# Kernel tuning notes

Measured on AMD Instinct MI355X. Metric: run time of the kernel, lower is better.

Reference implementation:

```python
import jax, jax.numpy as jnp
import numpy as np

B, S, D = 2, 2048, 2048
H = 16
HD = D // H  # 128


def setup_inputs() -> dict:
    key = jax.random.key(0)
    ks = jax.random.split(key, 9)
    s = 1.0 / np.sqrt(D)
    return {
        "hidden_states": jax.random.normal(ks[0], (B, S, D), dtype=jnp.float32),
        "Wq": jax.random.normal(ks[1], (D, D), dtype=jnp.float32) * s,
        "bq": jnp.zeros((D,), dtype=jnp.float32),
        "Wk": jax.random.normal(ks[2], (D, D), dtype=jnp.float32) * s,
        "bk": jnp.zeros((D,), dtype=jnp.float32),
        "Wv": jax.random.normal(ks[3], (D, D), dtype=jnp.float32) * s,
        "bv": jnp.zeros((D,), dtype=jnp.float32),
        "Wo": jax.random.normal(ks[4], (D, D), dtype=jnp.float32) * s,
        "bo": jnp.zeros((D,), dtype=jnp.float32),
    }


def reference(hidden_states, Wq, bq, Wk, bk, Wv, bv, Wo, bo):
    x = hidden_states
    # linear projections (torch Linear: x @ W.T + b)
    q = x @ Wq.T + bq
    k = x @ Wk.T + bk
    v = x @ Wv.T + bv
    # [B, S, H, HD] -> [B, H, S, HD]
    q = q.reshape(B, S, H, HD).transpose(0, 2, 1, 3)
    k = k.reshape(B, S, H, HD).transpose(0, 2, 1, 3)
    v = v.reshape(B, S, H, HD).transpose(0, 2, 1, 3)
    q = q / jnp.sqrt(jnp.float32(HD))
    # scores [B, H, S, S]
    scores = jnp.einsum("bhqd,bhkd->bhqk", q, k)
    causal = jnp.triu(jnp.full((S, S), -jnp.inf, dtype=scores.dtype), k=1)
    scores = scores + causal
    attn = jax.nn.softmax(scores, axis=-1)
    out = jnp.einsum("bhqk,bhkd->bhqd", attn, v)
    out = out.transpose(0, 2, 1, 3).reshape(B, S, D)
    return out @ Wo.T + bo
```

## Files before the change

kernel.cpp:

```cpp
#include <hip/hip_runtime.h>
#include <stdint.h>

#define S_LEN 2048
#define DMODEL 2048
#define NHEAD 16
#define HDIM 128

typedef __attribute__((ext_vector_type(8))) short short8;
typedef __attribute__((ext_vector_type(4))) float floatx4;

__device__ __forceinline__ unsigned short f2b(float f) {
  union { float f; unsigned u; } v; v.f = f;
  unsigned r = v.u + 0x7FFFu + ((v.u >> 16) & 1u);
  return (unsigned short)(r >> 16);
}

__device__ __forceinline__ void load_lds16(const unsigned short* g, unsigned short* l) {
  __builtin_amdgcn_global_load_lds((const __attribute__((address_space(1))) void*)g,
                                   (__attribute__((address_space(3))) void*)l, 16, 0, 0);
}

__global__ __launch_bounds__(256) void cvt_all(const float* __restrict__ x,
                                               const float* __restrict__ Wq, const float* __restrict__ Wk,
                                               const float* __restrict__ Wv, const float* __restrict__ Wo,
                                               unsigned short* __restrict__ xb,
                                               unsigned short* __restrict__ Wqb, unsigned short* __restrict__ Wkb,
                                               unsigned short* __restrict__ Wvb, unsigned short* __restrict__ Wob) {
  const size_t idx = (size_t)blockIdx.x * 256 + threadIdx.x;
  const int y = blockIdx.y;
  const float4* s; ushort4* d;
  if (y == 0)      { s = (const float4*)x;               d = (ushort4*)xb; }
  else if (y == 1) { s = (const float4*)x + (1u << 20);  d = (ushort4*)xb + (1u << 20); }
  else if (y == 2) { s = (const float4*)Wq;              d = (ushort4*)Wqb; }
  else if (y == 3) { s = (const float4*)Wk;              d = (ushort4*)Wkb; }
  else if (y == 4) { s = (const float4*)Wv;              d = (ushort4*)Wvb; }
  else             { s = (const float4*)Wo;              d = (ushort4*)Wob; }
  float4 f = s[idx];
  ushort4 o;
  o.x = f2b(f.x); o.y = f2b(f.y); o.z = f2b(f.z); o.w = f2b(f.w);
  d[idx] = o;
}

template <int MODE>
__global__ __launch_bounds__(256)
void gemm_bt(const unsigned short* __restrict__ A, const unsigned short* __restrict__ Bw,
             const float* __restrict__ bias, void* __restrict__ Cout,
             int M, int N, int K, float scale) {
  __shared__ unsigned short As[128 * 64];
  __shared__ unsigned short Bs[128 * 64];
  const int t = threadIdx.x;
  const int lane = t & 63, wave = t >> 6;
  const int quad = lane >> 4, lc = lane & 15;
  const int wm = wave >> 1, wn = wave & 1;
  const int m0 = blockIdx.y * 128, n0 = blockIdx.x * 128;

  const int srow = lane >> 3;
  const int skoff = ((lane & 7) ^ srow) * 8;
  const unsigned short* Ag[4];
  const unsigned short* Bg[4];
  unsigned short* Al[4];
  unsigned short* Bl[4];
#pragma unroll
  for (int i = 0; i < 4; i++) {
    int c = wave * 4 + i;
    Ag[i] = A + (size_t)(m0 + c * 8 + srow) * K + skoff;
    Bg[i] = Bw + (size_t)(n0 + c * 8 + srow) * K + skoff;
    Al[i] = &As[c * 512 + lane * 8];
    Bl[i] = &Bs[c * 512 + lane * 8];
  }

  int koff[2];
#pragma unroll
  for (int ks = 0; ks < 2; ks++) koff[ks] = ((ks * 4 + quad) ^ (lc & 7)) * 8;

  floatx4 acc[4][4] = {};

  for (int kt = 0; kt < K; kt += 64) {
    if (kt) __syncthreads();
#pragma unroll
    for (int i = 0; i < 4; i++) {
      load_lds16(Ag[i] + kt, Al[i]);
      load_lds16(Bg[i] + kt, Bl[i]);
    }
    __syncthreads();
#pragma unroll
    for (int ks = 0; ks < 2; ks++) {
      short8 av[4], bv[4];
#pragma unroll
      for (int mt = 0; mt < 4; mt++)
        av[mt] = *(const short8*)&As[(wm * 64 + mt * 16 + lc) * 64 + koff[ks]];
#pragma unroll
      for (int nt = 0; nt < 4; nt++)
        bv[nt] = *(const short8*)&Bs[(wn * 64 + nt * 16 + lc) * 64 + koff[ks]];
#pragma unroll
      for (int mt = 0; mt < 4; mt++)
#pragma unroll
        for (int nt = 0; nt < 4; nt++)
          acc[mt][nt] = __builtin_amdgcn_mfma_f32_16x16x32_bf16(av[mt], bv[nt], acc[mt][nt], 0, 0, 0);
    }
  }

#pragma unroll
  for (int nt = 0; nt < 4; nt++) {
    const int col = n0 + wn * 64 + nt * 16 + lc;
    const float bcol = bias[col];
#pragma unroll
    for (int mt = 0; mt < 4; mt++) {
      const int row0 = m0 + wm * 64 + mt * 16 + quad * 4;
      if (MODE == 1) {
        ushort4 o;
        o.x = f2b((acc[mt][nt][0] + bcol) * scale);
        o.y = f2b((acc[mt][nt][1] + bcol) * scale);
        o.z = f2b((acc[mt][nt][2] + bcol) * scale);
        o.w = f2b((acc[mt][nt][3] + bcol) * scale);
        int b = row0 >> 11;
        int s = row0 & (S_LEN - 1);
        *(ushort4*)&((unsigned short*)Cout)[((size_t)(b * DMODEL + col)) * S_LEN + s] = o;
      } else {
#pragma unroll
        for (int r = 0; r < 4; r++) {
          float v = (acc[mt][nt][r] + bcol) * scale;
          if (MODE == 2)
            ((float*)Cout)[(size_t)(row0 + r) * N + col] = v;
          else
            ((unsigned short*)Cout)[(size_t)(row0 + r) * N + col] = f2b(v);
        }
      }
    }
  }
}

__global__ __launch_bounds__(256, 2)
void attn_fwd(const unsigned short* __restrict__ Qg, const unsigned short* __restrict__ Kg,
              const unsigned short* __restrict__ Vtg, unsigned short* __restrict__ Og) {
  __shared__ unsigned short Ks[64 * 128];
  __shared__ unsigned short Vs[128 * 64];
  __shared__ unsigned short Ps[128 * 64];

  const int t = threadIdx.x;
  const int lane = t & 63, w = t >> 6;
  const int quad = lane >> 4, lc = lane & 15;
  const int y = blockIdx.y;
  const int tile = (y < 16) ? (int)blockIdx.x : 15 - (int)blockIdx.x;
  const int b = y >> 4, h = y & 15;
  const size_t qkbase = (size_t)b * S_LEN * DMODEL + h * HDIM;
  const size_t vtbase = ((size_t)(b * DMODEL + h * HDIM)) * S_LEN;
  const int q0 = tile * 128;
  const int wrow = q0 + w * 32;

  short8 aq[2][4];
#pragma unroll
  for (int pm = 0; pm < 2; pm++)
#pragma unroll
    for (int ks = 0; ks < 4; ks++)
      aq[pm][ks] = *(const short8*)&Qg[qkbase + (size_t)(wrow + pm * 16 + lc) * DMODEL + ks * 32 + quad * 8];

  const unsigned short* kga[4];
  const unsigned short* vga[4];
  unsigned short* klds[4];
  unsigned short* vlds[4];
#pragma unroll
  for (int i = 0; i < 4; i++) {
    int c = w * 4 + i;
    int krow = 4 * c + (lane >> 4);
    int kch = (lane & 15) ^ (krow & 15);
    kga[i] = Kg + qkbase + (size_t)krow * DMODEL + kch * 8;
    klds[i] = &Ks[c * 512 + lane * 8];
    int vrow = 8 * c + (lane >> 3);
    int vch = (lane & 7) ^ (vrow & 7);
    vga[i] = Vtg + vtbase + (size_t)vrow * S_LEN + vch * 8;
    vlds[i] = &Vs[c * 512 + lane * 8];
  }

  floatx4 oacc[2][8] = {};
  float m_run[2][4], l_run[2][4];
#pragma unroll
  for (int pm = 0; pm < 2; pm++)
#pragma unroll
    for (int r = 0; r < 4; r++) { m_run[pm][r] = -1e30f; l_run[pm][r] = 0.f; }

  const int kiters = 2 * tile + 2;
  for (int kb = 0; kb < kiters; kb++) {
    const int k0 = kb * 64;
    if (kb) __syncthreads();
#pragma unroll
    for (int i = 0; i < 4; i++) {
      load_lds16(kga[i] + (size_t)k0 * DMODEL, klds[i]);
      load_lds16(vga[i] + k0, vlds[i]);
    }
    __syncthreads();

    if (k0 <= wrow + 31) {
      floatx4 sacc[2][4] = {};
#pragma unroll
      for (int ks = 0; ks < 4; ks++) {
        short8 bk[4];
#pragma unroll
        for (int nt = 0; nt < 4; nt++) {
          int n = nt * 16 + lc;
          bk[nt] = *(const short8*)&Ks[n * 128 + (((ks * 4 + quad) ^ (n & 15)) * 8)];
        }
#pragma unroll
        for (int pm = 0; pm < 2; pm++)
#pragma unroll
          for (int nt = 0; nt < 4; nt++)
            sacc[pm][nt] = __builtin_amdgcn_mfma_f32_16x16x32_bf16(aq[pm][ks], bk[nt], sacc[pm][nt], 0, 0, 0);
      }

      float mx[2][4];
#pragma unroll
      for (int pm = 0; pm < 2; pm++)
#pragma unroll
        for (int r = 0; r < 4; r++) mx[pm][r] = -1e30f;
      if (k0 + 63 > wrow) {
#pragma unroll
        for (int pm = 0; pm < 2; pm++)
#pragma unroll
          for (int nt = 0; nt < 4; nt++) {
            int col = k0 + nt * 16 + lc;
#pragma unroll
            for (int r = 0; r < 4; r++) {
              if (col > wrow + pm * 16 + quad * 4 + r) sacc[pm][nt][r] = -1e30f;
              mx[pm][r] = fmaxf(mx[pm][r], sacc[pm][nt][r]);
            }
          }
      } else {
#pragma unroll
        for (int pm = 0; pm < 2; pm++)
#pragma unroll
          for (int nt = 0; nt < 4; nt++)
#pragma unroll
            for (int r = 0; r < 4; r++) mx[pm][r] = fmaxf(mx[pm][r], sacc[pm][nt][r]);
      }
#pragma unroll
      for (int off = 1; off < 16; off <<= 1)
#pragma unroll
        for (int pm = 0; pm < 2; pm++)
#pragma unroll
          for (int r = 0; r < 4; r++) mx[pm][r] = fmaxf(mx[pm][r], __shfl_xor(mx[pm][r], off));

      float alpha[2][4];
#pragma unroll
      for (int pm = 0; pm < 2; pm++)
#pragma unroll
        for (int r = 0; r < 4; r++) {
          float mnew = fmaxf(m_run[pm][r], mx[pm][r]);
          alpha[pm][r] = __expf(m_run[pm][r] - mnew);
          m_run[pm][r] = mnew;
          l_run[pm][r] *= alpha[pm][r];
        }
#pragma unroll
      for (int pm = 0; pm < 2; pm++)
#pragma unroll
        for (int nt = 0; nt < 4; nt++) {
          int chs = ((nt * 2 + (lc >> 3)) * 8) + (lc & 7);
#pragma unroll
          for (int r = 0; r < 4; r++) {
            float p = __expf(sacc[pm][nt][r] - m_run[pm][r]);
            l_run[pm][r] += p;
            int row = w * 32 + pm * 16 + quad * 4 + r;
            int sw = (((nt * 2 + (lc >> 3)) ^ (row & 7)) * 8) + (lc & 7);
            Ps[row * 64 + sw] = f2b(p);
          }
          (void)chs;
        }

#pragma unroll
      for (int pm = 0; pm < 2; pm++)
#pragma unroll
        for (int nt8 = 0; nt8 < 8; nt8++)
#pragma unroll
          for (int r = 0; r < 4; r++) oacc[pm][nt8][r] *= alpha[pm][r];

#pragma unroll
      for (int ks = 0; ks < 2; ks++) {
        short8 ap[2];
#pragma unroll
        for (int pm = 0; pm < 2; pm++) {
          int m = w * 32 + pm * 16 + lc;
          ap[pm] = *(const short8*)&Ps[m * 64 + (((ks * 4 + quad) ^ (m & 7)) * 8)];
        }
#pragma unroll
        for (int nt8 = 0; nt8 < 8; nt8++) {
          int n = nt8 * 16 + lc;
          short8 bv = *(const short8*)&Vs[n * 64 + (((ks * 4 + quad) ^ (n & 7)) * 8)];
#pragma unroll
          for (int pm = 0; pm < 2; pm++)
            oacc[pm][nt8] = __builtin_amdgcn_mfma_f32_16x16x32_bf16(ap[pm], bv, oacc[pm][nt8], 0, 0, 0);
        }
      }
    }
  }

#pragma unroll
  for (int off = 1; off < 16; off <<= 1)
#pragma unroll
    for (int pm = 0; pm < 2; pm++)
#pragma unroll
      for (int r = 0; r < 4; r++) l_run[pm][r] += __shfl_xor(l_run[pm][r], off);
#pragma unroll
  for (int pm = 0; pm < 2; pm++)
#pragma unroll
    for (int r = 0; r < 4; r++) {
      float inv = 1.f / l_run[pm][r];
      size_t obase = ((size_t)(b * S_LEN + wrow + pm * 16 + quad * 4 + r)) * DMODEL + h * HDIM;
#pragma unroll
      for (int nt8 = 0; nt8 < 8; nt8++)
        Og[obase + nt8 * 16 + lc] = f2b(oacc[pm][nt8][r] * inv);
    }
}

extern "C" void kernel_launch(void* const* d_in, const int* in_sizes, int n_in,
                              void* d_out, int out_size, void* d_ws, size_t ws_size,
                              hipStream_t stream) {
  const float* x  = (const float*)d_in[0];
  const float* Wq = (const float*)d_in[1];
  const float* bq = (const float*)d_in[2];
  const float* Wk = (const float*)d_in[3];
  const float* bk = (const float*)d_in[4];
  const float* Wv = (const float*)d_in[5];
  const float* bv = (const float*)d_in[6];
  const float* Wo = (const float*)d_in[7];
  const float* bo = (const float*)d_in[8];

  const int M = 2 * S_LEN;
  const int N = DMODEL, K = DMODEL;

  char* w = (char*)d_ws;
  unsigned short* xb  = (unsigned short*)(w);
  unsigned short* Wqb = (unsigned short*)(w + (size_t)16 * (1 << 20));
  unsigned short* Wkb = (unsigned short*)(w + (size_t)24 * (1 << 20));
  unsigned short* Wvb = (unsigned short*)(w + (size_t)32 * (1 << 20));
  unsigned short* Wob = (unsigned short*)(w + (size_t)40 * (1 << 20));
  unsigned short* Qb  = (unsigned short*)(w + (size_t)48 * (1 << 20));
  unsigned short* Kb  = (unsigned short*)(w + (size_t)64 * (1 << 20));
  unsigned short* Vtb = (unsigned short*)(w + (size_t)80 * (1 << 20));
  unsigned short* Ob  = (unsigned short*)(w + (size_t)96 * (1 << 20));

  cvt_all<<<dim3(4096, 6), 256, 0, stream>>>(x, Wq, Wk, Wv, Wo, xb, Wqb, Wkb, Wvb, Wob);

  dim3 gg(N / 128, M / 128);
  const float qscale = 0.08838834764831843f;
  gemm_bt<0><<<gg, 256, 0, stream>>>(xb, Wqb, bq, Qb, M, N, K, qscale);
  gemm_bt<0><<<gg, 256, 0, stream>>>(xb, Wkb, bk, Kb, M, N, K, 1.f);
  gemm_bt<1><<<gg, 256, 0, stream>>>(xb, Wvb, bv, Vtb, M, N, K, 1.f);

  attn_fwd<<<dim3(16, 32), 256, 0, stream>>>(Qb, Kb, Vtb, Ob);

  gemm_bt<2><<<gg, 256, 0, stream>>>(Ob, Wob, bo, d_out, M, N, K, 1.f);
}
```

Before: 411.3 us.

## Double-buffer K tiles and overlap V load with QK^T in attention

The attention kernel now double-buffers the K tile in shared memory and prefetches the next K block while computing QK^T on the current one. The V tile load is issued at the start of each iteration and waited on with a partial vmcnt wait plus a barrier just before the PV product. Softmax switches to exp2, with log2(e) folded into the Q projection scale. This aims to hide global-to-LDS load latency behind the MFMA work and to cut exp cost, at the price of more LDS use, which may reduce occupancy, and of a hand-written waitcnt whose count has to be right.

```diff
diff --git a/kernel.cpp b/kernel.cpp
--- a/kernel.cpp
+++ b/kernel.cpp
@@ -133,7 +133,7 @@
 __global__ __launch_bounds__(256, 2)
 void attn_fwd(const unsigned short* __restrict__ Qg, const unsigned short* __restrict__ Kg,
               const unsigned short* __restrict__ Vtg, unsigned short* __restrict__ Og) {
-  __shared__ unsigned short Ks[64 * 128];
+  __shared__ unsigned short Ks[2][64 * 128];
   __shared__ unsigned short Vs[128 * 64];
   __shared__ unsigned short Ps[128 * 64];
 
@@ -157,19 +157,16 @@
 
   const unsigned short* kga[4];
   const unsigned short* vga[4];
-  unsigned short* klds[4];
-  unsigned short* vlds[4];
+  int kloff[4], vloff[4];
 #pragma unroll
   for (int i = 0; i < 4; i++) {
     int c = w * 4 + i;
     int krow = 4 * c + (lane >> 4);
-    int kch = (lane & 15) ^ (krow & 15);
-    kga[i] = Kg + qkbase + (size_t)krow * DMODEL + kch * 8;
-    klds[i] = &Ks[c * 512 + lane * 8];
+    kga[i] = Kg + qkbase + (size_t)krow * DMODEL + ((lane & 15) ^ (krow & 15)) * 8;
+    kloff[i] = c * 512 + lane * 8;
     int vrow = 8 * c + (lane >> 3);
-    int vch = (lane & 7) ^ (vrow & 7);
-    vga[i] = Vtg + vtbase + (size_t)vrow * S_LEN + vch * 8;
-    vlds[i] = &Vs[c * 512 + lane * 8];
+    vga[i] = Vtg + vtbase + (size_t)vrow * S_LEN + ((lane & 7) ^ (vrow & 7)) * 8;
+    vloff[i] = c * 512 + lane * 8;
   }
 
   floatx4 oacc[2][8] = {};
@@ -180,25 +177,38 @@
     for (int r = 0; r < 4; r++) { m_run[pm][r] = -1e30f; l_run[pm][r] = 0.f; }
 
   const int kiters = 2 * tile + 2;
+
+#pragma unroll
+  for (int i = 0; i < 4; i++) load_lds16(kga[i], &Ks[0][kloff[i]]);
+
   for (int kb = 0; kb < kiters; kb++) {
     const int k0 = kb * 64;
-    if (kb) __syncthreads();
-#pragma unroll
-    for (int i = 0; i < 4; i++) {
-      load_lds16(kga[i] + (size_t)k0 * DMODEL, klds[i]);
-      load_lds16(vga[i] + k0, vlds[i]);
-    }
+    const int cur = kb & 1;
     __syncthreads();
 
-    if (k0 <= wrow + 31) {
-      floatx4 sacc[2][4] = {};
+#pragma unroll
+    for (int i = 0; i < 4; i++) load_lds16(vga[i] + k0, &Vs[vloff[i]]);
+    {
+      const size_t knext = (size_t)((kb + 1 < kiters) ? k0 + 64 : k0) * DMODEL;
+#pragma unroll
+      for (int i = 0; i < 4; i++) load_lds16(kga[i] + knext, &Ks[cur ^ 1][kloff[i]]);
+    }
+
+    const bool hasw = (k0 <= wrow + 31);
+    floatx4 sacc[2][4];
+    float alpha[2][4];
+    if (hasw) {
+#pragma unroll
+      for (int pm = 0; pm < 2; pm++)
+#pragma unroll
+        for (int nt = 0; nt < 4; nt++) sacc[pm][nt] = (floatx4){0.f, 0.f, 0.f, 0.f};
 #pragma unroll
       for (int ks = 0; ks < 4; ks++) {
         short8 bk[4];
 #pragma unroll
         for (int nt = 0; nt < 4; nt++) {
           int n = nt * 16 + lc;
-          bk[nt] = *(const short8*)&Ks[n * 128 + (((ks * 4 + quad) ^ (n & 15)) * 8)];
+          bk[nt] = *(const short8*)&Ks[cur][n * 128 + (((ks * 4 + quad) ^ (n & 15)) * 8)];
         }
 #pragma unroll
         for (int pm = 0; pm < 2; pm++)
@@ -239,13 +249,12 @@
 #pragma unroll
           for (int r = 0; r < 4; r++) mx[pm][r] = fmaxf(mx[pm][r], __shfl_xor(mx[pm][r], off));
 
-      float alpha[2][4];
 #pragma unroll
       for (int pm = 0; pm < 2; pm++)
 #pragma unroll
         for (int r = 0; r < 4; r++) {
           float mnew = fmaxf(m_run[pm][r], mx[pm][r]);
-          alpha[pm][r] = __expf(m_run[pm][r] - mnew);
+          alpha[pm][r] = __builtin_amdgcn_exp2f(m_run[pm][r] - mnew);
           m_run[pm][r] = mnew;
           l_run[pm][r] *= alpha[pm][r];
         }
@@ -253,18 +262,20 @@
       for (int pm = 0; pm < 2; pm++)
 #pragma unroll
         for (int nt = 0; nt < 4; nt++) {
-          int chs = ((nt * 2 + (lc >> 3)) * 8) + (lc & 7);
 #pragma unroll
           for (int r = 0; r < 4; r++) {
-            float p = __expf(sacc[pm][nt][r] - m_run[pm][r]);
+            float p = __builtin_amdgcn_exp2f(sacc[pm][nt][r] - m_run[pm][r]);
             l_run[pm][r] += p;
             int row = w * 32 + pm * 16 + quad * 4 + r;
             int sw = (((nt * 2 + (lc >> 3)) ^ (row & 7)) * 8) + (lc & 7);
             Ps[row * 64 + sw] = f2b(p);
           }
-          (void)chs;
-        }
-
+        }
+    }
+
+    asm volatile("s_waitcnt vmcnt(4)\n\ts_barrier" ::: "memory");
+
+    if (hasw) {
 #pragma unroll
       for (int pm = 0; pm < 2; pm++)
 #pragma unroll
@@ -340,7 +351,7 @@
   cvt_all<<<dim3(4096, 6), 256, 0, stream>>>(x, Wq, Wk, Wv, Wo, xb, Wqb, Wkb, Wvb, Wob);
 
   dim3 gg(N / 128, M / 128);
-  const float qscale = 0.08838834764831843f;
+  const float qscale = 0.08838834764831843f * 1.4426950408889634f;
   gemm_bt<0><<<gg, 256, 0, stream>>>(xb, Wqb, bq, Qb, M, N, K, qscale);
   gemm_bt<0><<<gg, 256, 0, stream>>>(xb, Wkb, bk, Kb, M, N, K, 1.f);
   gemm_bt<1><<<gg, 256, 0, stream>>>(xb, Wvb, bv, Vtb, M, N, K, 1.f);
```

Measured after the change: 396.5 us. 3.6% less time.
